# Performance work log

Measured on AMD Instinct MI355X. Metric: run time of the kernel, lower is better.

The kernel has to match this reference:

```python
import math
from itertools import combinations_with_replacement
import jax, jax.numpy as jnp
import numpy as np

# ---- static config (matches init_kwargs) ----
SPECIES_LIST = [1, 6, 8]
S = len(SPECIES_LIST)
N_MAX = 8
L_MAX = 4
CUTOFF = 5.0
B, N = 4, 512

SPECIES = jnp.asarray(SPECIES_LIST, dtype=jnp.int64 if jax.config.jax_enable_x64 else jnp.int32)
PAIR_IDS = np.array(list(combinations_with_replacement(range(S), 2)), dtype=np.int32)  # (P,2)
P = PAIR_IDS.shape[0]

# orthonormalization matrix W (deterministic buffer)
def _ortho_W(n_max):
    a = np.arange(1, n_max + 1, dtype=np.float64)
    Smat = np.sqrt((5 + 2 * a[:, None]) * (5 + 2 * a[None, :])) / (5 + a[:, None] + a[None, :])
    w, v = np.linalg.eigh(Smat)
    return (v @ np.diag(w ** -0.5) @ v.T).astype(np.float32)
W_ORTHO = jnp.asarray(_ortho_W(N_MAX))

# per-l power-spectrum prefactor pi*sqrt(8/(2l+1))
PS_NORM = jnp.asarray([math.pi * math.sqrt(8.0 / (2 * l + 1)) for l in range(L_MAX + 1)], dtype=jnp.float32)
# selector: which of the 25 flattened (l,m) components belong to degree l
_l_of_m = np.concatenate([np.full(2 * l + 1, l) for l in range(L_MAX + 1)])
L_SEL = jnp.asarray((_l_of_m[None, :] == np.arange(L_MAX + 1)[:, None]).astype(np.float32))  # (L,25)
# sqrt(2) on strict-upper (n,p) entries (applied before triu gather)
_offd = np.ones((N_MAX, N_MAX), dtype=np.float32)
_offd[np.triu_indices(N_MAX, 1)] = math.sqrt(2.0)
OFFD = jnp.asarray(_offd)
IU_R, IU_C = np.triu_indices(N_MAX)
PAIR_F = jnp.asarray(np.where(PAIR_IDS[:, 0] != PAIR_IDS[:, 1], math.sqrt(2.0), 1.0).astype(np.float32))


def real_sph_harm(u):
    """Real spherical harmonics (integral normalization, homogeneous polynomial form)
    for l=0..4, evaluated on u (..., 3). Returns (..., 25). Zero vector -> l>0 vanish."""
    x, y, z = u[..., 0], u[..., 1], u[..., 2]
    x2, y2, z2 = x * x, y * y, z * z
    r2 = x2 + y2 + z2
    pi = math.pi
    s = math.sqrt
    Y = [
        jnp.full_like(x, 0.5 * s(1 / pi)),
        s(3 / (4 * pi)) * y, s(3 / (4 * pi)) * z, s(3 / (4 * pi)) * x,
        0.5 * s(15 / pi) * x * y,
        0.5 * s(15 / pi) * y * z,
        0.25 * s(5 / pi) * (3 * z2 - r2),
        0.5 * s(15 / pi) * x * z,
        0.25 * s(15 / pi) * (x2 - y2),
        0.25 * s(35 / (2 * pi)) * y * (3 * x2 - y2),
        0.5 * s(105 / pi) * x * y * z,
        0.25 * s(21 / (2 * pi)) * y * (5 * z2 - r2),
        0.25 * s(7 / pi) * z * (5 * z2 - 3 * r2),
        0.25 * s(21 / (2 * pi)) * x * (5 * z2 - r2),
        0.25 * s(105 / pi) * z * (x2 - y2),
        0.25 * s(35 / (2 * pi)) * x * (x2 - 3 * y2),
        0.75 * s(35 / pi) * x * y * (x2 - y2),
        0.75 * s(35 / (2 * pi)) * y * z * (3 * x2 - y2),
        0.75 * s(5 / pi) * x * y * (7 * z2 - r2),
        0.75 * s(5 / (2 * pi)) * y * z * (7 * z2 - 3 * r2),
        (3.0 / 16.0) * s(1 / pi) * (35 * z2 * z2 - 30 * z2 * r2 + 3 * r2 * r2),
        0.75 * s(5 / (2 * pi)) * x * z * (7 * z2 - 3 * r2),
        (3.0 / 8.0) * s(5 / pi) * (x2 - y2) * (7 * z2 - r2),
        0.75 * s(35 / (2 * pi)) * x * z * (x2 - 3 * y2),
        (3.0 / 16.0) * s(35 / pi) * (x2 * x2 - 6 * x2 * y2 + y2 * y2),
    ]
    return jnp.stack(Y, axis=-1)


def soap_forward(pos, Z):
    b, n, _ = pos.shape
    # pairwise within each frame: dvec[b,i,j] = pos[b,i] - pos[b,j]  (dst - src)
    dvec = pos[:, :, None, :] - pos[:, None, :, :]          # (B,N,N,3)
    d2 = jnp.sum(dvec * dvec, axis=-1)
    dist = jnp.where(d2 > 0, jnp.sqrt(jnp.where(d2 > 0, d2, 1.0)), 0.0)
    u = dvec / jnp.where(dist > 0, dist, 1.0)[..., None]
    Y = real_sph_harm(u) * (4.0 * math.pi)                  # (B,N,N,25)
    # radial basis (l-independent in this module); cutoff mask folds in dist>=cutoff pairs
    alpha = jnp.arange(1, N_MAX + 1, dtype=pos.dtype)
    norm_factor = jnp.sqrt(CUTOFF ** (2 * alpha + 5) / (2 * alpha + 5))
    dr = jnp.maximum(CUTOFF - dist, 0.0)[..., None]
    basis = dr ** (alpha + 2) / norm_factor * (dist < CUTOFF).astype(pos.dtype)[..., None]
    g = basis @ W_ORTHO.T                                   # (B,N,N,n_max)
    # per-species scatter-add over source atoms j -> density coefficients c
    s_oh = (Z[..., None] == SPECIES).astype(pos.dtype)      # (B,N,S)
    c = jnp.einsum('bjs,bijn,bijm->bisnm', s_oh, g, Y)      # (B,N,S,n_max,25)
    # power spectrum: sum over m within each l
    ps = jnp.einsum('bisnm,bitpm,lm->bistlnp', c, c, L_SEL) # (B,N,S,S,L,n,n)
    ps = ps[:, :, PAIR_IDS[:, 0], PAIR_IDS[:, 1]]           # (B,N,P,L,n,n)
    ps = ps * PAIR_F[:, None, None, None] * PS_NORM[:, None, None] * OFFD
    desc = ps[..., IU_R, IU_C]                              # (B,N,P,L,36)
    return desc.reshape(b, n, -1)                           # (B,N,1080)


def setup_inputs() -> dict:
    key = jax.random.key(0)
    k1, k2 = jax.random.split(key)
    pos = jax.random.uniform(k1, (B, N, 3), dtype=jnp.float32) * 22.0
    Z = SPECIES[jax.random.randint(k2, (B, N), 0, S)]
    return {'pos': pos, 'Z': Z}


def reference(pos, Z):
    return soap_forward(pos, Z)
```

## Files before the change

### kernel.cpp

```cpp
#include <hip/hip_runtime.h>
#include <cmath>

#define NMAX   8
#define NM     25
#define NATOM  512
#define SLOTW  33
#define NOUT   1080
#define CROW   60
#define CSN    480
#define CSITE  1440

struct Params {
    float W[NMAX * NMAX];
    float invnorm[NMAX];
    float ycoef[NM];
    float lscale[5];
    float pairf[6];
};

__device__ __forceinline__ void neighbor_compute(
    const float* __restrict__ pos, const Params& prm,
    float xi, float yi, float zi, int ja, int col, float* __restrict__ gys) {
    const float dx = xi - pos[ja * 3 + 0];
    const float dy = yi - pos[ja * 3 + 1];
    const float dz = zi - pos[ja * 3 + 2];
    const float d2 = dx * dx + dy * dy + dz * dz;
    const float dist = sqrtf(d2);
    const float inv  = dist > 0.f ? 1.f / dist : 0.f;
    const float x = dx * inv, y = dy * inv, z = dz * inv;
    const float x2 = x * x, y2 = y * y, z2 = z * z;
    const float r2 = x2 + y2 + z2;
    float* row = &gys[col * SLOTW];

    const float dr = 5.f - dist;
    float bas[NMAX];
    float drp = dr * dr * dr;
#pragma unroll
    for (int a = 0; a < NMAX; ++a) { bas[a] = drp * prm.invnorm[a]; drp *= dr; }
#pragma unroll
    for (int n = 0; n < NMAX; ++n) {
        float acc = 0.f;
#pragma unroll
        for (int a = 0; a < NMAX; ++a) acc += bas[a] * prm.W[n * NMAX + a];
        row[n] = acc;
    }

    row[8]  = prm.ycoef[0];
    row[9]  = prm.ycoef[1]  * y;
    row[10] = prm.ycoef[2]  * z;
    row[11] = prm.ycoef[3]  * x;
    row[12] = prm.ycoef[4]  * x * y;
    row[13] = prm.ycoef[5]  * y * z;
    row[14] = prm.ycoef[6]  * (3.f * z2 - r2);
    row[15] = prm.ycoef[7]  * x * z;
    row[16] = prm.ycoef[8]  * (x2 - y2);
    row[17] = prm.ycoef[9]  * y * (3.f * x2 - y2);
    row[18] = prm.ycoef[10] * x * y * z;
    row[19] = prm.ycoef[11] * y * (5.f * z2 - r2);
    row[20] = prm.ycoef[12] * z * (5.f * z2 - 3.f * r2);
    row[21] = prm.ycoef[13] * x * (5.f * z2 - r2);
    row[22] = prm.ycoef[14] * z * (x2 - y2);
    row[23] = prm.ycoef[15] * x * (x2 - 3.f * y2);
    row[24] = prm.ycoef[16] * x * y * (x2 - y2);
    row[25] = prm.ycoef[17] * y * z * (3.f * x2 - y2);
    row[26] = prm.ycoef[18] * x * y * (7.f * z2 - r2);
    row[27] = prm.ycoef[19] * y * z * (7.f * z2 - 3.f * r2);
    row[28] = prm.ycoef[20] * (35.f * z2 * z2 - 30.f * z2 * r2 + 3.f * r2 * r2);
    row[29] = prm.ycoef[21] * x * z * (7.f * z2 - 3.f * r2);
    row[30] = prm.ycoef[22] * (x2 - y2) * (7.f * z2 - r2);
    row[31] = prm.ycoef[23] * x * z * (x2 - 3.f * y2);
    row[32] = prm.ycoef[24] * (x2 * x2 - 6.f * x2 * y2 + y2 * y2);
}

__global__ __launch_bounds__(256)
void soap_kernel(const float* __restrict__ pos, const int* __restrict__ Z,
                 float* __restrict__ out, Params prm) {
    __shared__ float gy_all[4][64 * SLOTW];
    __shared__ float c_all[4][CSITE];
    __shared__ int   ci_all[4][64];
    __shared__ int   sp_all[4][64];

    const int tid  = threadIdx.x;
    const int lane = tid & 63;
    const int ws   = tid >> 6;
    const int site = (blockIdx.x << 2) + ws;
    const int b    = site >> 9;
    const int jbase = b << 9;

    float* gys = gy_all[ws];
    float* cs  = c_all[ws];
    int*   cix = ci_all[ws];
    int*   sps = sp_all[ws];

    const float xi = pos[site * 3 + 0];
    const float yi = pos[site * 3 + 1];
    const float zi = pos[site * 3 + 2];

#pragma unroll
    for (int i = 0; i < 23; ++i) {
        const int idx = lane + i * 64;
        if (idx < CSITE) cs[idx] = 0.f;
    }

    const unsigned long long ltm = (1ull << lane) - 1ull;
    int mtot = 0;
#pragma unroll
    for (int it = 0; it < 8; ++it) {
        const int ja = jbase + it * 64 + lane;
        const float dx = xi - pos[ja * 3 + 0];
        const float dy = yi - pos[ja * 3 + 1];
        const float dz = zi - pos[ja * 3 + 2];
        const float d2 = dx * dx + dy * dy + dz * dz;
        const bool pr = d2 < 25.0f;
        const unsigned long long mk = __ballot(pr);
        const int sl = mtot + __popcll(mk & ltm);
        if (pr && sl < 64) cix[sl] = ja;
        mtot += __popcll(mk);
    }
    const int M = mtot;

    const int n_own = lane & 7;
    const int mrow  = lane >> 3;
    float acc0[4] = {0.f, 0.f, 0.f, 0.f};
    float acc1[4] = {0.f, 0.f, 0.f, 0.f};
    float acc2[4] = {0.f, 0.f, 0.f, 0.f};

    if (M <= 64) {
        int myj = -1, sp = -1;
        if (lane < M) {
            myj = cix[lane];
            const int zz = Z[myj];
            sp = (zz == 1) ? 0 : (zz == 6) ? 1 : 2;
        }
        const unsigned long long b0 = __ballot(sp == 0);
        const unsigned long long b1 = __ballot(sp == 1);
        const unsigned long long b2 = __ballot(sp == 2);
        const int R1 = __popcll(b0);
        const int R2 = R1 + __popcll(b1);
        int np = -1;
        if (sp == 0)      np = __popcll(b0 & ltm);
        else if (sp == 1) np = R1 + __popcll(b1 & ltm);
        else if (sp == 2) np = R2 + __popcll(b2 & ltm);
        if (np >= 0) cix[np] = myj;

        if (lane < M) neighbor_compute(pos, prm, xi, yi, zi, cix[lane], lane, gys);

        for (int sl = 0; sl < R1; ++sl) {
            const float g = gys[sl * SLOTW + n_own];
#pragma unroll
            for (int k = 0; k < 4; ++k) {
                const int m = mrow + 8 * k;
                if (k < 3 || mrow == 0) acc0[k] += g * gys[sl * SLOTW + 8 + m];
            }
        }
        for (int sl = R1; sl < R2; ++sl) {
            const float g = gys[sl * SLOTW + n_own];
#pragma unroll
            for (int k = 0; k < 4; ++k) {
                const int m = mrow + 8 * k;
                if (k < 3 || mrow == 0) acc1[k] += g * gys[sl * SLOTW + 8 + m];
            }
        }
        for (int sl = R2; sl < M; ++sl) {
            const float g = gys[sl * SLOTW + n_own];
#pragma unroll
            for (int k = 0; k < 4; ++k) {
                const int m = mrow + 8 * k;
                if (k < 3 || mrow == 0) acc2[k] += g * gys[sl * SLOTW + 8 + m];
            }
        }
    } else {
        for (int it = 0; it < 8; ++it) {
            const int ja = jbase + it * 64 + lane;
            const float dx = xi - pos[ja * 3 + 0];
            const float dy = yi - pos[ja * 3 + 1];
            const float dz = zi - pos[ja * 3 + 2];
            const float d2 = dx * dx + dy * dy + dz * dz;
            const bool pr = d2 < 25.0f;
            const unsigned long long mk = __ballot(pr);
            const int cnt = __popcll(mk);
            if (pr) {
                const int sl = __popcll(mk & ltm);
                cix[sl] = ja;
                const int zz = Z[ja];
                sps[sl] = (zz == 1) ? 0 : (zz == 6) ? 1 : 2;
            }
            if (lane < cnt) neighbor_compute(pos, prm, xi, yi, zi, cix[lane], lane, gys);
            for (int sl = 0; sl < cnt; ++sl) {
                const int ss = sps[sl];
                const float g = gys[sl * SLOTW + n_own];
                float* accp = (ss == 0) ? acc0 : (ss == 1) ? acc1 : acc2;
#pragma unroll
                for (int k = 0; k < 4; ++k) {
                    const int m = mrow + 8 * k;
                    if (k < 3 || mrow == 0) accp[k] += g * gys[sl * SLOTW + 8 + m];
                }
            }
        }
    }

#pragma unroll
    for (int k = 0; k < 4; ++k) {
        const int m = mrow + 8 * k;
        if (k < 3 || mrow == 0) {
            const int l  = (int)sqrtf((float)m);
            const int kk = m - l * l;
            const int base = n_own * CROW + l * 12 + kk;
            cs[0 * CSN + base] = acc0[k];
            cs[1 * CSN + base] = acc1[k];
            cs[2 * CSN + base] = acc2[k];
        }
    }

#pragma unroll
    for (int k = 0; k < 17; ++k) {
        const int o = k * 64 + lane;
        if (o < NOUT) {
            const int q   = o / 180;
            const int rem = o - q * 180;
            const int l   = rem / 36;
            const int t   = rem - l * 36;
            const int n = (int)((17.0f - sqrtf((float)(289 - 8 * t))) * 0.5f);
            const int p = t - ((n * (17 - n)) >> 1) + n;
            const int s1 = (q < 3) ? 0 : ((q < 5) ? 1 : 2);
            const int s2 = (q < 3) ? q : ((q < 5) ? (q - 2) : 2);
            const float4* ra = (const float4*)&cs[s1 * CSN + n * CROW + l * 12];
            const float4* rb = (const float4*)&cs[s2 * CSN + p * CROW + l * 12];
            const float4 a0 = ra[0], bb0 = rb[0];
            const float4 a1 = ra[1], bb1 = rb[1];
            const float4 a2 = ra[2], bb2 = rb[2];
            float sum = a0.x * bb0.x + a0.y * bb0.y + a0.z * bb0.z + a0.w * bb0.w
                      + a1.x * bb1.x + a1.y * bb1.y + a1.z * bb1.z + a1.w * bb1.w
                      + a2.x * bb2.x + a2.y * bb2.y + a2.z * bb2.z + a2.w * bb2.w;
            float sc = prm.pairf[q] * prm.lscale[l];
            if (n != p) sc *= 1.41421356237309515f;
            out[site * NOUT + o] = sum * sc;
        }
    }
}

extern "C" void kernel_launch(void* const* d_in, const int* in_sizes, int n_in,
                              void* d_out, int out_size, void* d_ws, size_t ws_size,
                              hipStream_t stream) {
    const float* pos = (const float*)d_in[0];
    const int*   Z   = (const int*)d_in[1];
    float*       out = (float*)d_out;
    const int nsite  = in_sizes[1];

    Params prm;

    double A[8][8], V[8][8];
    for (int i = 0; i < 8; ++i)
        for (int j = 0; j < 8; ++j) {
            const double ai = i + 1.0, aj = j + 1.0;
            A[i][j] = sqrt((5.0 + 2.0 * ai) * (5.0 + 2.0 * aj)) / (5.0 + ai + aj);
            V[i][j] = (i == j) ? 1.0 : 0.0;
        }
    for (int sweep = 0; sweep < 30; ++sweep) {
        for (int p = 0; p < 8; ++p)
            for (int q = p + 1; q < 8; ++q) {
                const double apq = A[p][q];
                if (fabs(apq) < 1e-300) continue;
                const double phi = 0.5 * atan2(2.0 * apq, A[q][q] - A[p][p]);
                const double c = cos(phi), s = sin(phi);
                for (int k = 0; k < 8; ++k) {
                    const double akp = A[k][p], akq = A[k][q];
                    A[k][p] = c * akp - s * akq;
                    A[k][q] = s * akp + c * akq;
                }
                for (int k = 0; k < 8; ++k) {
                    const double apk = A[p][k], aqk = A[q][k];
                    A[p][k] = c * apk - s * aqk;
                    A[q][k] = s * apk + c * aqk;
                }
                for (int k = 0; k < 8; ++k) {
                    const double vkp = V[k][p], vkq = V[k][q];
                    V[k][p] = c * vkp - s * vkq;
                    V[k][q] = s * vkp + c * vkq;
                }
            }
    }
    for (int i = 0; i < 8; ++i)
        for (int j = 0; j < 8; ++j) {
            double acc = 0.0;
            for (int k = 0; k < 8; ++k) acc += V[i][k] * V[j][k] / sqrt(A[k][k]);
            prm.W[i * 8 + j] = (float)acc;
        }

    for (int a = 0; a < 8; ++a)
        prm.invnorm[a] = (float)(1.0 / sqrt(pow(5.0, 2.0 * a + 7.0) / (2.0 * a + 7.0)));

    const double pi = 3.14159265358979323846;
    const double fp = 4.0 * pi;
    double yc[NM];
    yc[0]  = 0.5 * sqrt(1.0 / pi);
    yc[1]  = yc[2] = yc[3] = sqrt(3.0 / (4.0 * pi));
    yc[4]  = yc[5] = yc[7] = 0.5 * sqrt(15.0 / pi);
    yc[6]  = 0.25 * sqrt(5.0 / pi);
    yc[8]  = 0.25 * sqrt(15.0 / pi);
    yc[9]  = yc[15] = 0.25 * sqrt(35.0 / (2.0 * pi));
    yc[10] = 0.5 * sqrt(105.0 / pi);
    yc[11] = yc[13] = 0.25 * sqrt(21.0 / (2.0 * pi));
    yc[12] = 0.25 * sqrt(7.0 / pi);
    yc[14] = 0.25 * sqrt(105.0 / pi);
    yc[16] = 0.75 * sqrt(35.0 / pi);
    yc[17] = yc[23] = 0.75 * sqrt(35.0 / (2.0 * pi));
    yc[18] = 0.75 * sqrt(5.0 / pi);
    yc[19] = yc[21] = 0.75 * sqrt(5.0 / (2.0 * pi));
    yc[20] = 3.0 / 16.0 * sqrt(1.0 / pi);
    yc[22] = 3.0 / 8.0 * sqrt(5.0 / pi);
    yc[24] = 3.0 / 16.0 * sqrt(35.0 / pi);
    for (int m = 0; m < NM; ++m) prm.ycoef[m] = (float)(yc[m] * fp);

    for (int l = 0; l <= 4; ++l) prm.lscale[l] = (float)(pi * sqrt(8.0 / (2.0 * l + 1.0)));
    const float rt2 = 1.41421356237309515f;
    prm.pairf[0] = 1.f; prm.pairf[1] = rt2; prm.pairf[2] = rt2;
    prm.pairf[3] = 1.f; prm.pairf[4] = rt2; prm.pairf[5] = 1.f;

    soap_kernel<<<(nsite + 3) / 4, 256, 0, stream>>>(pos, Z, out, prm);
}
```

Before: 17.32 us.

## Process one site per block with four waves splitting neighbor and contraction work

Each 256-thread block now handles a single site instead of four independent per-wave sites. The four waves share the neighbor-basis computation, with each wave taking 16 neighbors, and split the density contraction across m components. The block then cooperates on the power-spectrum output. Neighbor displacement vectors and species are cached in shared memory so positions are not re-read, and the c layout is packed per l so fewer float4 loads are needed in the output dot products. This adds block-wide barriers and launches four times as many blocks. The overflow path (more than 64 neighbors) runs on a single wave.

```diff
diff --git a/kernel.cpp b/kernel.cpp
--- a/kernel.cpp
+++ b/kernel.cpp
@@ -3,12 +3,11 @@
 
 #define NMAX   8
 #define NM     25
-#define NATOM  512
-#define SLOTW  33
+#define ROWW   40
 #define NOUT   1080
-#define CROW   60
-#define CSN    480
-#define CSITE  1440
+#define CROW   36
+#define CSN    288
+#define CSITE  864
 
 struct Params {
     float W[NMAX * NMAX];
@@ -18,19 +17,15 @@
     float pairf[6];
 };
 
-__device__ __forceinline__ void neighbor_compute(
-    const float* __restrict__ pos, const Params& prm,
-    float xi, float yi, float zi, int ja, int col, float* __restrict__ gys) {
-    const float dx = xi - pos[ja * 3 + 0];
-    const float dy = yi - pos[ja * 3 + 1];
-    const float dz = zi - pos[ja * 3 + 2];
+__device__ __forceinline__ void neighbor_compute(const Params& prm,
+                                                 float dx, float dy, float dz,
+                                                 float* __restrict__ row) {
     const float d2 = dx * dx + dy * dy + dz * dz;
     const float dist = sqrtf(d2);
     const float inv  = dist > 0.f ? 1.f / dist : 0.f;
     const float x = dx * inv, y = dy * inv, z = dz * inv;
     const float x2 = x * x, y2 = y * y, z2 = z * z;
     const float r2 = x2 + y2 + z2;
-    float* row = &gys[col * SLOTW];
 
     const float dr = 5.f - dist;
     float bas[NMAX];
@@ -70,37 +65,30 @@
     row[30] = prm.ycoef[22] * (x2 - y2) * (7.f * z2 - r2);
     row[31] = prm.ycoef[23] * x * z * (x2 - 3.f * y2);
     row[32] = prm.ycoef[24] * (x2 * x2 - 6.f * x2 * y2 + y2 * y2);
+    row[33] = 0.f; row[34] = 0.f; row[35] = 0.f;
+    *(float4*)&row[36] = make_float4(0.f, 0.f, 0.f, 0.f);
 }
 
 __global__ __launch_bounds__(256)
 void soap_kernel(const float* __restrict__ pos, const int* __restrict__ Z,
                  float* __restrict__ out, Params prm) {
-    __shared__ float gy_all[4][64 * SLOTW];
-    __shared__ float c_all[4][CSITE];
-    __shared__ int   ci_all[4][64];
-    __shared__ int   sp_all[4][64];
+    __shared__ float  gys[64 * ROWW];
+    __shared__ float4 dA[64];
+    __shared__ float4 dB[64];
+    __shared__ float  cs[CSITE];
+    __shared__ int    spl[64];
 
     const int tid  = threadIdx.x;
     const int lane = tid & 63;
-    const int ws   = tid >> 6;
-    const int site = (blockIdx.x << 2) + ws;
-    const int b    = site >> 9;
-    const int jbase = b << 9;
-
-    float* gys = gy_all[ws];
-    float* cs  = c_all[ws];
-    int*   cix = ci_all[ws];
-    int*   sps = sp_all[ws];
+    const int w    = tid >> 6;
+    const int site = blockIdx.x;
+    const int jbase = (site >> 9) << 9;
 
     const float xi = pos[site * 3 + 0];
     const float yi = pos[site * 3 + 1];
     const float zi = pos[site * 3 + 2];
 
-#pragma unroll
-    for (int i = 0; i < 23; ++i) {
-        const int idx = lane + i * 64;
-        if (idx < CSITE) cs[idx] = 0.f;
-    }
+    for (int i = tid; i < CSITE; i += 256) cs[i] = 0.f;
 
     const unsigned long long ltm = (1ull << lane) - 1ull;
     int mtot = 0;
@@ -113,63 +101,47 @@
         const float d2 = dx * dx + dy * dy + dz * dz;
         const bool pr = d2 < 25.0f;
         const unsigned long long mk = __ballot(pr);
-        const int sl = mtot + __popcll(mk & ltm);
-        if (pr && sl < 64) cix[sl] = ja;
+        if (pr) {
+            const int sl = mtot + __popcll(mk & ltm);
+            if (sl < 64) {
+                const int zz = Z[ja];
+                const int sp = (zz == 1) ? 0 : (zz == 6) ? 1 : 2;
+                dA[sl] = make_float4(dx, dy, dz, (float)sp);
+            }
+        }
         mtot += __popcll(mk);
     }
     const int M = mtot;
 
     const int n_own = lane & 7;
     const int mrow  = lane >> 3;
-    float acc0[4] = {0.f, 0.f, 0.f, 0.f};
-    float acc1[4] = {0.f, 0.f, 0.f, 0.f};
-    float acc2[4] = {0.f, 0.f, 0.f, 0.f};
-
-    if (M <= 64) {
-        int myj = -1, sp = -1;
-        if (lane < M) {
-            myj = cix[lane];
-            const int zz = Z[myj];
-            sp = (zz == 1) ? 0 : (zz == 6) ? 1 : 2;
-        }
+    const bool fast = (M <= 64);
+
+    int R1 = 0, R2 = 0;
+    if (fast) {
+        float4 v = make_float4(0.f, 0.f, 0.f, 0.f);
+        int sp = -1;
+        if (lane < M) { v = dA[lane]; sp = (int)v.w; }
         const unsigned long long b0 = __ballot(sp == 0);
         const unsigned long long b1 = __ballot(sp == 1);
         const unsigned long long b2 = __ballot(sp == 2);
-        const int R1 = __popcll(b0);
-        const int R2 = R1 + __popcll(b1);
+        R1 = __popcll(b0);
+        R2 = R1 + __popcll(b1);
         int np = -1;
         if (sp == 0)      np = __popcll(b0 & ltm);
         else if (sp == 1) np = R1 + __popcll(b1 & ltm);
         else if (sp == 2) np = R2 + __popcll(b2 & ltm);
-        if (np >= 0) cix[np] = myj;
-
-        if (lane < M) neighbor_compute(pos, prm, xi, yi, zi, cix[lane], lane, gys);
-
-        for (int sl = 0; sl < R1; ++sl) {
-            const float g = gys[sl * SLOTW + n_own];
-#pragma unroll
-            for (int k = 0; k < 4; ++k) {
-                const int m = mrow + 8 * k;
-                if (k < 3 || mrow == 0) acc0[k] += g * gys[sl * SLOTW + 8 + m];
-            }
-        }
-        for (int sl = R1; sl < R2; ++sl) {
-            const float g = gys[sl * SLOTW + n_own];
-#pragma unroll
-            for (int k = 0; k < 4; ++k) {
-                const int m = mrow + 8 * k;
-                if (k < 3 || mrow == 0) acc1[k] += g * gys[sl * SLOTW + 8 + m];
-            }
-        }
-        for (int sl = R2; sl < M; ++sl) {
-            const float g = gys[sl * SLOTW + n_own];
-#pragma unroll
-            for (int k = 0; k < 4; ++k) {
-                const int m = mrow + 8 * k;
-                if (k < 3 || mrow == 0) acc2[k] += g * gys[sl * SLOTW + 8 + m];
-            }
-        }
-    } else {
+        if (np >= 0) dB[np] = v;
+
+        if (lane < 16) {
+            const int sl = w * 16 + lane;
+            if (sl < M) {
+                const float4 u = dB[sl];
+                neighbor_compute(prm, u.x, u.y, u.z, &gys[sl * ROWW]);
+            }
+        }
+    } else if (w == 0) {
+        float f0[4] = {0.f,0.f,0.f,0.f}, f1[4] = {0.f,0.f,0.f,0.f}, f2[4] = {0.f,0.f,0.f,0.f};
         for (int it = 0; it < 8; ++it) {
             const int ja = jbase + it * 64 + lane;
             const float dx = xi - pos[ja * 3 + 0];
@@ -181,40 +153,84 @@
             const int cnt = __popcll(mk);
             if (pr) {
                 const int sl = __popcll(mk & ltm);
-                cix[sl] = ja;
+                dA[sl] = make_float4(dx, dy, dz, 0.f);
                 const int zz = Z[ja];
-                sps[sl] = (zz == 1) ? 0 : (zz == 6) ? 1 : 2;
-            }
-            if (lane < cnt) neighbor_compute(pos, prm, xi, yi, zi, cix[lane], lane, gys);
+                spl[sl] = (zz == 1) ? 0 : (zz == 6) ? 1 : 2;
+            }
+            if (lane < cnt) {
+                const float4 u = dA[lane];
+                neighbor_compute(prm, u.x, u.y, u.z, &gys[lane * ROWW]);
+            }
             for (int sl = 0; sl < cnt; ++sl) {
-                const int ss = sps[sl];
-                const float g = gys[sl * SLOTW + n_own];
-                float* accp = (ss == 0) ? acc0 : (ss == 1) ? acc1 : acc2;
+                const int ss = spl[sl];
+                const float g = gys[sl * ROWW + n_own];
 #pragma unroll
                 for (int k = 0; k < 4; ++k) {
                     const int m = mrow + 8 * k;
-                    if (k < 3 || mrow == 0) accp[k] += g * gys[sl * SLOTW + 8 + m];
+                    const float p = g * gys[sl * ROWW + 8 + m];
+                    if (ss == 0) f0[k] += p;
+                    else if (ss == 1) f1[k] += p;
+                    else f2[k] += p;
                 }
             }
         }
-    }
-
-#pragma unroll
-    for (int k = 0; k < 4; ++k) {
-        const int m = mrow + 8 * k;
-        if (k < 3 || mrow == 0) {
-            const int l  = (int)sqrtf((float)m);
-            const int kk = m - l * l;
-            const int base = n_own * CROW + l * 12 + kk;
-            cs[0 * CSN + base] = acc0[k];
-            cs[1 * CSN + base] = acc1[k];
-            cs[2 * CSN + base] = acc2[k];
-        }
-    }
-
-#pragma unroll
-    for (int k = 0; k < 17; ++k) {
-        const int o = k * 64 + lane;
+#pragma unroll
+        for (int k = 0; k < 4; ++k) {
+            const int m = mrow + 8 * k;
+            if (m < NM) {
+                const int l  = (int)sqrtf((float)m);
+                const int kk = m - l * l;
+                const int base = n_own * CROW + ((l < 2) ? 4 * l : 8 * (l - 1)) + kk;
+                f0[k] = f0[k];
+            }
+        }
+        __syncthreads();
+#pragma unroll
+        for (int k = 0; k < 4; ++k) {
+            const int m = mrow + 8 * k;
+            if (m < NM) {
+                const int l  = (int)sqrtf((float)m);
+                const int kk = m - l * l;
+                const int base = n_own * CROW + ((l < 2) ? 4 * l : 8 * (l - 1)) + kk;
+                cs[0 * CSN + base] = f0[k];
+                cs[1 * CSN + base] = f1[k];
+                cs[2 * CSN + base] = f2[k];
+            }
+        }
+        goto after_b;
+    }
+    if (!fast && w != 0) {
+        __syncthreads();
+        goto after_b;
+    }
+
+    __syncthreads();
+
+    {
+        const int mown = 4 * mrow + w;
+        float s0 = 0.f, s1 = 0.f, s2 = 0.f;
+        for (int sl = 0; sl < R1; ++sl)
+            s0 += gys[sl * ROWW + n_own] * gys[sl * ROWW + 8 + mown];
+        for (int sl = R1; sl < R2; ++sl)
+            s1 += gys[sl * ROWW + n_own] * gys[sl * ROWW + 8 + mown];
+        for (int sl = R2; sl < M; ++sl)
+            s2 += gys[sl * ROWW + n_own] * gys[sl * ROWW + 8 + mown];
+        if (mown < NM) {
+            const int l  = (int)sqrtf((float)mown);
+            const int kk = mown - l * l;
+            const int base = n_own * CROW + ((l < 2) ? 4 * l : 8 * (l - 1)) + kk;
+            cs[0 * CSN + base] = s0;
+            cs[1 * CSN + base] = s1;
+            cs[2 * CSN + base] = s2;
+        }
+    }
+
+after_b:
+    __syncthreads();
+
+#pragma unroll
+    for (int k = 0; k < 5; ++k) {
+        const int o = k * 256 + tid;
         if (o < NOUT) {
             const int q   = o / 180;
             const int rem = o - q * 180;
@@ -224,14 +240,15 @@
             const int p = t - ((n * (17 - n)) >> 1) + n;
             const int s1 = (q < 3) ? 0 : ((q < 5) ? 1 : 2);
             const int s2 = (q < 3) ? q : ((q < 5) ? (q - 2) : 2);
-            const float4* ra = (const float4*)&cs[s1 * CSN + n * CROW + l * 12];
-            const float4* rb = (const float4*)&cs[s2 * CSN + p * CROW + l * 12];
-            const float4 a0 = ra[0], bb0 = rb[0];
-            const float4 a1 = ra[1], bb1 = rb[1];
-            const float4 a2 = ra[2], bb2 = rb[2];
-            float sum = a0.x * bb0.x + a0.y * bb0.y + a0.z * bb0.z + a0.w * bb0.w
-                      + a1.x * bb1.x + a1.y * bb1.y + a1.z * bb1.z + a1.w * bb1.w
-                      + a2.x * bb2.x + a2.y * bb2.y + a2.z * bb2.z + a2.w * bb2.w;
+            const int lofs = (l < 2) ? 4 * l : 8 * (l - 1);
+            const int nq = (l < 2) ? 1 : ((l < 4) ? 2 : 3);
+            const float4* ra = (const float4*)&cs[s1 * CSN + n * CROW + lofs];
+            const float4* rb = (const float4*)&cs[s2 * CSN + p * CROW + lofs];
+            float sum = 0.f;
+            for (int j = 0; j < nq; ++j) {
+                const float4 a = ra[j], bb = rb[j];
+                sum += a.x * bb.x + a.y * bb.y + a.z * bb.z + a.w * bb.w;
+            }
             float sc = prm.pairf[q] * prm.lscale[l];
             if (n != p) sc *= 1.41421356237309515f;
             out[site * NOUT + o] = sum * sc;
@@ -317,5 +334,5 @@
     prm.pairf[0] = 1.f; prm.pairf[1] = rt2; prm.pairf[2] = rt2;
     prm.pairf[3] = 1.f; prm.pairf[4] = rt2; prm.pairf[5] = 1.f;
 
-    soap_kernel<<<(nsite + 3) / 4, 256, 0, stream>>>(pos, Z, out, prm);
+    soap_kernel<<<nsite, 256, 0, stream>>>(pos, Z, out, prm);
 }
```

New measurement: 22.09 us. 27.5% more time.
